# Optimization experiments

Hardware: AMD Instinct MI355X
Metric: run time of the kernel (lower is better)

Reference implementation:

```python
import jax, jax.numpy as jnp
import numpy as np

B, S, E, H = 4, 2048, 1024, 16
HD = E // H  # head_dim = 64


def setup_inputs() -> dict:
    key = jax.random.key(0)
    k1, k2, k3, k4 = jax.random.split(key, 4)
    x = jax.random.normal(k1, (B, S, E), dtype=jnp.float32)
    Wqkv = jax.random.normal(k2, (3 * E, E), dtype=jnp.float32) * (E ** -0.5)
    Wo = jax.random.normal(k3, (E, E), dtype=jnp.float32) * (E ** -0.5)
    bo = jax.random.normal(k4, (E,), dtype=jnp.float32) * 0.01
    return {"x": x, "Wqkv": Wqkv, "Wo": Wo, "bo": bo}


def reference(x, Wqkv, Wo, bo):
    b, s, e = x.shape
    # qkv projection (nn.Linear without bias: x @ W^T) -> (b, s, 3e)
    qkv = x @ Wqkv.T
    # reshape (b, s, H, 3*HD) -> (b, H, s, 3*HD), then chunk into q,k,v
    qkv = qkv.reshape(b, s, H, 3 * HD).transpose(0, 2, 1, 3)
    q, k, v = jnp.split(qkv, 3, axis=-1)  # each (b, H, s, HD)
    scale = 1.0 / jnp.sqrt(jnp.asarray(HD, dtype=x.dtype))
    scores = jnp.einsum('bhqd,bhkd->bhqk', q, k) * scale  # (b, H, s, s)
    causal = jnp.tril(jnp.ones((s, s), dtype=bool))
    scores = jnp.where(causal, scores, -jnp.inf)
    probs = jax.nn.softmax(scores, axis=-1)
    out = jnp.einsum('bhqk,bhkd->bhqd', probs, v)  # (b, H, s, HD)
    out = out.transpose(0, 2, 1, 3).reshape(b, s, e)
    return out @ Wo.T + bo
```

## Files before the change

kernel.cpp:

```cpp
#include <hip/hip_runtime.h>
#include <stdint.h>

#define Bn 4
#define Sn 2048
#define En 1024
#define Hn 16
#define HDn 64

typedef __bf16 bf16;
typedef __bf16 bf16x4 __attribute__((ext_vector_type(4)));
typedef __bf16 bf16x8 __attribute__((ext_vector_type(8)));
typedef float  f32x4  __attribute__((ext_vector_type(4)));
typedef float  f32x16 __attribute__((ext_vector_type(16)));
typedef uint32_t u32x4 __attribute__((ext_vector_type(4)));

#define GLDS(gp, lp) __builtin_amdgcn_global_load_lds( \
    (const __attribute__((address_space(1))) void*)(gp), \
    (__attribute__((address_space(3))) void*)(lp), 16, 0, 0)

#define BAR() __builtin_amdgcn_s_barrier()
#define WLG() do { asm volatile("s_waitcnt lgkmcnt(0)" ::: "memory"); \
                   __builtin_amdgcn_sched_barrier(0); } while (0)
#define WVM4() asm volatile("s_waitcnt vmcnt(4)" ::: "memory")

__global__ __launch_bounds__(256) void cvt_f32_to_bf16(
    const float* __restrict__ in, bf16* __restrict__ out, int n4)
{
    int i = blockIdx.x * 256 + threadIdx.x;
    if (i >= n4) return;
    float4 f = reinterpret_cast<const float4*>(in)[i];
    bf16x4 o;
    o[0] = (bf16)f.x; o[1] = (bf16)f.y; o[2] = (bf16)f.z; o[3] = (bf16)f.w;
    reinterpret_cast<bf16x4*>(out)[i] = o;
}

template<int MODE>
__global__ __launch_bounds__(512, 2) void gemm256(
    const bf16* __restrict__ Ag, const bf16* __restrict__ Bw,
    int M, int N, int K,
    bf16* __restrict__ q_out, bf16* __restrict__ k_out, bf16* __restrict__ v_out,
    float* __restrict__ c_out, const float* __restrict__ bias)
{
    __shared__ __align__(16) bf16 lA[2 * 256 * 64];
    __shared__ __align__(16) bf16 lB[2 * 256 * 64];

    const int tid  = threadIdx.x;
    const int lane = tid & 63;
    const int w    = tid >> 6;
    const int wm = w >> 2, wn = w & 3;
    const int lr = lane & 15, lg = lane >> 4;
    const int m0 = blockIdx.y * 256;
    const int n0 = blockIdx.x * 256;
    const int NT = K >> 6;
    const int niter = NT >> 1;

    const int srow = tid >> 3;
    const int sck  = (tid & 7) ^ ((tid >> 3) & 7);

    f32x4 acc[8][4] = {};

    auto stageA = [&](int t, int half) {
        const int ts = t < NT ? t : NT - 1;
        bf16* Ld = lA + ((t & 1) ? 16384 : 0) + (half*128 + w*8) * 64;
        const bf16* S = Ag + (size_t)(m0 + half*128 + srow) * K + ts*64 + sck*8;
        GLDS(S, Ld);
        GLDS(S + (size_t)64 * K, Ld + 64 * 64);
    };
    auto stageB = [&](int t, int half) {
        const int ts = t < NT ? t : NT - 1;
        bf16* Ld = lB + ((t & 1) ? 16384 : 0) + (half*128 + w*8) * 64;
        const bf16* S = Bw + (size_t)(n0 + half*128 + srow) * K + ts*64 + sck*8;
        GLDS(S, Ld);
        GLDS(S + (size_t)64 * K, Ld + 64 * 64);
    };
    auto ldA4 = [&](bf16x8 (&a)[4][2], const bf16* Lb, int qm) {
        #pragma unroll
        for (int ii = 0; ii < 4; ++ii) {
            const bf16* p = Lb + (wm*128 + qm*64 + ii*16 + lr) * 64;
            #pragma unroll
            for (int kk = 0; kk < 2; ++kk)
                a[ii][kk] = *reinterpret_cast<const bf16x8*>(p + (((kk << 2) + lg) ^ (lr & 7)) * 8);
        }
    };
    auto ldB2 = [&](bf16x8 (&b)[2][2], const bf16* Lb, int qn) {
        #pragma unroll
        for (int j = 0; j < 2; ++j) {
            const bf16* p = Lb + (wn*64 + qn*32 + j*16 + lr) * 64;
            #pragma unroll
            for (int kk = 0; kk < 2; ++kk)
                b[j][kk] = *reinterpret_cast<const bf16x8*>(p + (((kk << 2) + lg) ^ (lr & 7)) * 8);
        }
    };
    auto mmac = [&](const bf16x8 (&a)[4][2], const bf16x8 (&b)[2][2], int qm, int qn) {
        __builtin_amdgcn_s_setprio(1);
        #pragma unroll
        for (int ii = 0; ii < 4; ++ii)
            #pragma unroll
            for (int j = 0; j < 2; ++j)
                #pragma unroll
                for (int kk = 0; kk < 2; ++kk)
                    acc[qm*4 + ii][qn*2 + j] = __builtin_amdgcn_mfma_f32_16x16x32_bf16(
                        a[ii][kk], b[j][kk], acc[qm*4 + ii][qn*2 + j], 0, 0, 0);
        __builtin_amdgcn_s_setprio(0);
    };

    stageA(0, 0); stageA(0, 1); stageB(0, 0); stageB(0, 1);
    stageB(1, 0); stageB(1, 1);
    WVM4(); BAR();

    const bf16* A0 = lA;          const bf16* A1 = lA + 16384;
    const bf16* B0l = lB;         const bf16* B1l = lB + 16384;
    bf16x8 a[4][2], b0[2][2], b1[2][2];

    for (int i = 0; i < niter; ++i) {
        const int t = 2 * i;
        ldA4(a, A0, 0); ldB2(b0, B0l, 0);
        stageA(t + 1, 0);
        BAR(); WLG();
        mmac(a, b0, 0, 0);
        BAR();
        ldB2(b1, B0l, 1);
        stageA(t + 1, 1);
        BAR(); WLG();
        mmac(a, b1, 0, 1);
        BAR();
        ldA4(a, A0, 1);
        stageB(t + 2, 0);
        BAR(); WLG();
        mmac(a, b0, 1, 0);
        BAR();
        stageB(t + 2, 1);
        WVM4(); BAR();
        mmac(a, b1, 1, 1);
        BAR();
        ldA4(a, A1, 0); ldB2(b0, B1l, 0);
        stageA(t + 2, 0);
        BAR(); WLG();
        mmac(a, b0, 0, 0);
        BAR();
        ldB2(b1, B1l, 1);
        stageA(t + 2, 1);
        BAR(); WLG();
        mmac(a, b1, 0, 1);
        BAR();
        ldA4(a, A1, 1);
        stageB(t + 3, 0);
        BAR(); WLG();
        mmac(a, b0, 1, 0);
        BAR();
        stageB(t + 3, 1);
        WVM4(); BAR();
        mmac(a, b1, 1, 1);
        BAR();
    }

    #pragma unroll
    for (int ii = 0; ii < 8; ++ii) {
        #pragma unroll
        for (int j = 0; j < 4; ++j) {
            const int colb = n0 + wn*64 + j*16 + lr;
            #pragma unroll
            for (int r = 0; r < 4; ++r) {
                const int rowb = m0 + wm*128 + ii*16 + lg*4 + r;
                const float v = acc[ii][j][r];
                if (MODE == 0) {
                    const int bb = rowb >> 11, s = rowb & (Sn - 1);
                    const int h = colb / 192, rr = colb - h*192;
                    const int wq = rr >> 6, hd = rr & 63;
                    const size_t off = (((size_t)(bb*Hn + h))*Sn + s)*HDn + hd;
                    const bf16 bv = (bf16)v;
                    if (wq == 0)      q_out[off] = bv;
                    else if (wq == 1) k_out[off] = bv;
                    else              v_out[off] = bv;
                } else {
                    c_out[(size_t)rowb*N + colb] = v + bias[colb];
                }
            }
        }
    }
}

template<int MODE>
__global__ __launch_bounds__(256) void gemm_bt(
    const bf16* __restrict__ A, const bf16* __restrict__ Bw,
    int M, int N, int K,
    bf16* __restrict__ q_out, bf16* __restrict__ k_out, bf16* __restrict__ v_out,
    float* __restrict__ c_out, const float* __restrict__ bias)
{
    __shared__ bf16 lA[128*64];
    __shared__ bf16 lB[128*64];
    const int tid  = threadIdx.x;
    const int lane = tid & 63;
    const int wv   = tid >> 6;
    const int wm = wv >> 1, wn = wv & 1;
    const int m0 = blockIdx.y * 128;
    const int n0 = blockIdx.x * 128;
    const int lr = lane & 15, lg = lane >> 4;

    f32x4 acc[4][4] = {};

    const int rowA = wv*8 + (lane>>3);
    const int col8 = (lane&7)*8;

    for (int k0 = 0; k0 < K; k0 += 64) {
        #pragma unroll
        for (int c = 0; c < 4; ++c) {
            int row = c*32 + rowA;
            GLDS(A  + (size_t)(m0+row)*K + k0 + col8, lA + (c*32 + wv*8)*64);
            GLDS(Bw + (size_t)(n0+row)*K + k0 + col8, lB + (c*32 + wv*8)*64);
        }
        __syncthreads();
        #pragma unroll
        for (int kk = 0; kk < 64; kk += 32) {
            bf16x8 af[4], bfv[4];
            #pragma unroll
            for (int i = 0; i < 4; ++i)
                af[i] = *reinterpret_cast<const bf16x8*>(lA + (wm*64 + i*16 + lr)*64 + kk + lg*8);
            #pragma unroll
            for (int j = 0; j < 4; ++j)
                bfv[j] = *reinterpret_cast<const bf16x8*>(lB + (wn*64 + j*16 + lr)*64 + kk + lg*8);
            #pragma unroll
            for (int i = 0; i < 4; ++i)
                #pragma unroll
                for (int j = 0; j < 4; ++j)
                    acc[i][j] = __builtin_amdgcn_mfma_f32_16x16x32_bf16(af[i], bfv[j], acc[i][j], 0, 0, 0);
        }
        __syncthreads();
    }

    #pragma unroll
    for (int i = 0; i < 4; ++i) {
        #pragma unroll
        for (int j = 0; j < 4; ++j) {
            const int colb = n0 + wn*64 + j*16 + lr;
            #pragma unroll
            for (int r = 0; r < 4; ++r) {
                const int rowb = m0 + wm*64 + i*16 + lg*4 + r;
                const float v = acc[i][j][r];
                if (MODE == 0) {
                    const int b = rowb >> 11, s = rowb & (Sn-1);
                    const int h = colb / 192, rr = colb - h*192;
                    const int wq = rr >> 6, hd = rr & 63;
                    const size_t off = (((size_t)(b*Hn + h))*Sn + s)*HDn + hd;
                    const bf16 bv = (bf16)v;
                    if (wq == 0)      q_out[off] = bv;
                    else if (wq == 1) k_out[off] = bv;
                    else              v_out[off] = bv;
                } else {
                    c_out[(size_t)rowb*N + colb] = v + bias[colb];
                }
            }
        }
    }
}

static __device__ __forceinline__ uint32_t pkbf(float lo, float hi)
{
    uint16_t a = __builtin_bit_cast(uint16_t, (bf16)lo);
    uint16_t b = __builtin_bit_cast(uint16_t, (bf16)hi);
    return (uint32_t)a | ((uint32_t)b << 16);
}

__global__ __launch_bounds__(512) void attn_fwd(
    const bf16* __restrict__ Q, const bf16* __restrict__ Kg, const bf16* __restrict__ Vg,
    bf16* __restrict__ O)
{
    __shared__ __align__(16) bf16 Kl[64*64];
    __shared__ __align__(16) bf16 Vt[64*64];

    const int tid  = threadIdx.x;
    const int lane = tid & 63;
    const int w    = tid >> 6;
    const int col  = lane & 31;
    const int hv   = lane >> 5;
    const int bh   = blockIdx.x;
    const int qb   = (gridDim.y - 1) - blockIdx.y;
    const int q0w  = qb*256 + w*32;
    const int qg   = q0w + col;

    const bf16* Qb = Q  + (size_t)bh*Sn*HDn;
    const bf16* Kb = Kg + (size_t)bh*Sn*HDn;
    const bf16* Vb = Vg + (size_t)bh*Sn*HDn;

    bf16x8 aq[4];
    #pragma unroll
    for (int ks = 0; ks < 4; ++ks)
        aq[ks] = *reinterpret_cast<const bf16x8*>(Qb + (size_t)qg*HDn + ks*16 + hv*8);

    f32x16 ov[2] = {};
    const float S2 = 0.18033688011112042f;
    float m_run = -1e30f, l_run = 0.f;

    const int srow = tid >> 3;
    const int scol = tid & 7;
    const int ksw  = scol ^ (srow & 7);

    const int nkt = 4*(qb+1);
    for (int kt = 0; kt < nkt; ++kt) {
        const int k0 = kt*64;
        __syncthreads();
        GLDS(Kb + (size_t)(k0 + srow)*HDn + ksw*8, Kl + (size_t)w*512);
        {
            bf16x8 vv = *reinterpret_cast<const bf16x8*>(Vb + (size_t)(k0 + srow)*HDn + scol*8);
            #pragma unroll
            for (int j = 0; j < 8; ++j) {
                const int chunk = (scol*8 + j)*8 + ((srow>>3) ^ scol);
                Vt[chunk*8 + (srow&7)] = vv[j];
            }
        }
        __syncthreads();

        if (k0 > q0w + 31) continue;

        f32x16 st[2] = {};
        #pragma unroll
        for (int kb = 0; kb < 2; ++kb) {
            const int key = kb*32 + col;
            #pragma unroll
            for (int ks = 0; ks < 4; ++ks) {
                const int chunk = key*8 + ((ks*2 + hv) ^ (key & 7));
                bf16x8 kf = *reinterpret_cast<const bf16x8*>(Kl + chunk*8);
                st[kb] = __builtin_amdgcn_mfma_f32_32x32x16_bf16(kf, aq[ks], st[kb], 0, 0, 0);
            }
        }

        if (k0 + 63 > q0w) {
            #pragma unroll
            for (int kb = 0; kb < 2; ++kb)
                #pragma unroll
                for (int r = 0; r < 16; ++r) {
                    const int keyg = k0 + kb*32 + (r&3) + 8*(r>>2) + 4*hv;
                    if (keyg > qg) st[kb][r] = -1e30f;
                }
        }

        float mx = st[0][0];
        #pragma unroll
        for (int kb = 0; kb < 2; ++kb)
            #pragma unroll
            for (int r = 0; r < 16; ++r)
                mx = fmaxf(mx, st[kb][r]);
        mx = fmaxf(mx, __shfl_xor(mx, 32));
        const float smax2 = mx * S2;

        if (!__all(smax2 - m_run <= 8.0f)) {
            const float mn = fmaxf(m_run, smax2);
            const float fr = exp2f(m_run - mn);
            l_run *= fr;
            #pragma unroll
            for (int hb = 0; hb < 2; ++hb)
                #pragma unroll
                for (int r = 0; r < 16; ++r)
                    ov[hb][r] *= fr;
            m_run = mn;
        }

        uint32_t wpk[2][8];
        float sum = 0.f;
        #pragma unroll
        for (int kb = 0; kb < 2; ++kb)
            #pragma unroll
            for (int i = 0; i < 8; ++i) {
                const float e0 = exp2f(fmaf(st[kb][2*i],   S2, -m_run));
                const float e1 = exp2f(fmaf(st[kb][2*i+1], S2, -m_run));
                sum += e0 + e1;
                wpk[kb][i] = pkbf(e0, e1);
            }
        l_run += sum;

        #pragma unroll
        for (int s = 0; s < 4; ++s) {
            const int kb = s >> 1, ls = s & 1;
            const uint32_t send0 = hv ? wpk[kb][4*ls+0] : wpk[kb][4*ls+2];
            const uint32_t send1 = hv ? wpk[kb][4*ls+1] : wpk[kb][4*ls+3];
            const uint32_t keep0 = hv ? wpk[kb][4*ls+2] : wpk[kb][4*ls+0];
            const uint32_t keep1 = hv ? wpk[kb][4*ls+3] : wpk[kb][4*ls+1];
            const uint32_t r0 = (uint32_t)__shfl_xor((int)send0, 32);
            const uint32_t r1 = (uint32_t)__shfl_xor((int)send1, 32);
            u32x4 pwv = { hv ? r0 : keep0, hv ? r1 : keep1,
                          hv ? keep0 : r0, hv ? keep1 : r1 };
            bf16x8 pB = __builtin_bit_cast(bf16x8, pwv);
            #pragma unroll
            for (int hb = 0; hb < 2; ++hb) {
                const int hd = hb*32 + col;
                const int chunk = hd*8 + ((s*2 + hv) ^ ((hd>>3) & 7));
                bf16x8 vf = *reinterpret_cast<const bf16x8*>(Vt + chunk*8);
                ov[hb] = __builtin_amdgcn_mfma_f32_32x32x16_bf16(vf, pB, ov[hb], 0, 0, 0);
            }
        }
    }

    const float lt  = l_run + __shfl_xor(l_run, 32);
    const float inv = 1.0f / lt;
    const int b = bh >> 4, hh = bh & 15;
    bf16* Ob = O + ((size_t)(b*Sn + qg))*En + hh*HDn;
    #pragma unroll
    for (int hb = 0; hb < 2; ++hb)
        #pragma unroll
        for (int g = 0; g < 4; ++g) {
            bf16x4 o4;
            #pragma unroll
            for (int r4 = 0; r4 < 4; ++r4)
                o4[r4] = (bf16)(ov[hb][g*4 + r4] * inv);
            *reinterpret_cast<bf16x4*>(Ob + hb*32 + g*8 + 4*hv) = o4;
        }
}

extern "C" void kernel_launch(void* const* d_in, const int* in_sizes, int n_in,
                              void* d_out, int out_size, void* d_ws, size_t ws_size,
                              hipStream_t stream)
{
    (void)in_sizes; (void)n_in; (void)out_size; (void)ws_size;
    const float* x    = (const float*)d_in[0];
    const float* Wqkv = (const float*)d_in[1];
    const float* Wo   = (const float*)d_in[2];
    const float* bo   = (const float*)d_in[3];
    float* out = (float*)d_out;

    const size_t nBS = (size_t)Bn*Sn;
    char* ws = (char*)d_ws;
    bf16* xb    = (bf16*)ws; ws += nBS*En*2;
    bf16* wqkvb = (bf16*)ws; ws += (size_t)3*En*En*2;
    bf16* wob   = (bf16*)ws; ws += (size_t)En*En*2;
    bf16* Qb    = (bf16*)ws; ws += nBS*En*2;
    bf16* Kb    = (bf16*)ws; ws += nBS*En*2;
    bf16* Vb    = (bf16*)ws; ws += nBS*En*2;
    bf16* AO    = (bf16*)ws; ws += nBS*En*2;

    int n4 = (int)(nBS*En/4);
    cvt_f32_to_bf16<<<(n4+255)/256, 256, 0, stream>>>(x, xb, n4);
    n4 = 3*En*En/4;
    cvt_f32_to_bf16<<<(n4+255)/256, 256, 0, stream>>>(Wqkv, wqkvb, n4);
    n4 = En*En/4;
    cvt_f32_to_bf16<<<(n4+255)/256, 256, 0, stream>>>(Wo, wob, n4);

    gemm256<0><<<dim3(3*En/256, nBS/256), 512, 0, stream>>>(
        xb, wqkvb, (int)nBS, 3*En, En, Qb, Kb, Vb, nullptr, nullptr);

    attn_fwd<<<dim3(Bn*Hn, Sn/256), 512, 0, stream>>>(Qb, Kb, Vb, AO);

    gemm_bt<1><<<dim3(En/128, nBS/128), 256, 0, stream>>>(
        AO, wob, (int)nBS, En, En, nullptr, nullptr, nullptr, out, bo);
}
```

Baseline: 197.1 us.

## Double-buffer K/V tiles in attention kernel and prefetch next tile during compute

The attention kernel now keeps two LDS buffers for K and transposed V. The loads for the next 64-key tile (async global-to-LDS for K, register load for V) are issued before the current tile's QK^T and softmax work, and the V transpose-store happens before the PV matmul. This cuts the per-iteration pair of barriers to a single one and hides global load latency behind MFMA work. It also raises MFMA wave priority with s_setprio, and in exchange doubles LDS use and keeps more registers live.

```diff
diff --git a/kernel.cpp b/kernel.cpp
--- a/kernel.cpp
+++ b/kernel.cpp
@@ -22,6 +22,7 @@
 #define WLG() do { asm volatile("s_waitcnt lgkmcnt(0)" ::: "memory"); \
                    __builtin_amdgcn_sched_barrier(0); } while (0)
 #define WVM4() asm volatile("s_waitcnt vmcnt(4)" ::: "memory")
+#define WVM0() asm volatile("s_waitcnt vmcnt(0)" ::: "memory")
 
 __global__ __launch_bounds__(256) void cvt_f32_to_bf16(
     const float* __restrict__ in, bf16* __restrict__ out, int n4)
@@ -265,8 +266,8 @@
     const bf16* __restrict__ Q, const bf16* __restrict__ Kg, const bf16* __restrict__ Vg,
     bf16* __restrict__ O)
 {
-    __shared__ __align__(16) bf16 Kl[64*64];
-    __shared__ __align__(16) bf16 Vt[64*64];
+    __shared__ __align__(16) bf16 Kl[2][64*64];
+    __shared__ __align__(16) bf16 Vt[2][64*64];
 
     const int tid  = threadIdx.x;
     const int lane = tid & 63;
@@ -295,99 +296,125 @@
     const int scol = tid & 7;
     const int ksw  = scol ^ (srow & 7);
 
+    auto vWrite = [&](bf16* Vd, bf16x8 vv) {
+        #pragma unroll
+        for (int j = 0; j < 8; ++j) {
+            const int chunk = (scol*8 + j)*8 + ((srow>>3) ^ scol);
+            Vd[chunk*8 + (srow&7)] = vv[j];
+        }
+    };
+
     const int nkt = 4*(qb+1);
+
+    GLDS(Kb + (size_t)srow*HDn + ksw*8, &Kl[0][0] + (size_t)w*512);
+    {
+        bf16x8 vv0 = *reinterpret_cast<const bf16x8*>(Vb + (size_t)srow*HDn + scol*8);
+        WVM0();
+        vWrite(&Vt[0][0], vv0);
+    }
+    __syncthreads();
+
     for (int kt = 0; kt < nkt; ++kt) {
+        const int cur = kt & 1;
         const int k0 = kt*64;
+        const bool more = (kt + 1 < nkt);
+        const bool skip = (k0 > q0w + 31);
+
+        bf16x8 vv;
+        if (more) {
+            GLDS(Kb + (size_t)(k0 + 64 + srow)*HDn + ksw*8, &Kl[cur^1][0] + (size_t)w*512);
+            vv = *reinterpret_cast<const bf16x8*>(Vb + (size_t)(k0 + 64 + srow)*HDn + scol*8);
+        }
+
+        uint32_t wpk[2][8];
+        if (!skip) {
+            f32x16 st[2] = {};
+            __builtin_amdgcn_s_setprio(1);
+            #pragma unroll
+            for (int kb = 0; kb < 2; ++kb) {
+                const int key = kb*32 + col;
+                #pragma unroll
+                for (int ks = 0; ks < 4; ++ks) {
+                    const int chunk = key*8 + ((ks*2 + hv) ^ (key & 7));
+                    bf16x8 kf = *reinterpret_cast<const bf16x8*>(&Kl[cur][0] + chunk*8);
+                    st[kb] = __builtin_amdgcn_mfma_f32_32x32x16_bf16(kf, aq[ks], st[kb], 0, 0, 0);
+                }
+            }
+            __builtin_amdgcn_s_setprio(0);
+
+            if (k0 + 63 > q0w) {
+                #pragma unroll
+                for (int kb = 0; kb < 2; ++kb)
+                    #pragma unroll
+                    for (int r = 0; r < 16; ++r) {
+                        const int keyg = k0 + kb*32 + (r&3) + 8*(r>>2) + 4*hv;
+                        if (keyg > qg) st[kb][r] = -1e30f;
+                    }
+            }
+
+            float mx = st[0][0];
+            #pragma unroll
+            for (int kb = 0; kb < 2; ++kb)
+                #pragma unroll
+                for (int r = 0; r < 16; ++r)
+                    mx = fmaxf(mx, st[kb][r]);
+            mx = fmaxf(mx, __shfl_xor(mx, 32));
+            const float smax2 = mx * S2;
+
+            if (!__all(smax2 - m_run <= 8.0f)) {
+                const float mn = fmaxf(m_run, smax2);
+                const float fr = exp2f(m_run - mn);
+                l_run *= fr;
+                #pragma unroll
+                for (int hb = 0; hb < 2; ++hb)
+                    #pragma unroll
+                    for (int r = 0; r < 16; ++r)
+                        ov[hb][r] *= fr;
+                m_run = mn;
+            }
+
+            float sum = 0.f;
+            #pragma unroll
+            for (int kb = 0; kb < 2; ++kb)
+                #pragma unroll
+                for (int i = 0; i < 8; ++i) {
+                    const float e0 = exp2f(fmaf(st[kb][2*i],   S2, -m_run));
+                    const float e1 = exp2f(fmaf(st[kb][2*i+1], S2, -m_run));
+                    sum += e0 + e1;
+                    wpk[kb][i] = pkbf(e0, e1);
+                }
+            l_run += sum;
+        }
+
+        WVM0();
+        if (more) vWrite(&Vt[cur^1][0], vv);
+
+        if (!skip) {
+            #pragma unroll
+            for (int s = 0; s < 4; ++s) {
+                const int kb = s >> 1, ls = s & 1;
+                const uint32_t send0 = hv ? wpk[kb][4*ls+0] : wpk[kb][4*ls+2];
+                const uint32_t send1 = hv ? wpk[kb][4*ls+1] : wpk[kb][4*ls+3];
+                const uint32_t keep0 = hv ? wpk[kb][4*ls+2] : wpk[kb][4*ls+0];
+                const uint32_t keep1 = hv ? wpk[kb][4*ls+3] : wpk[kb][4*ls+1];
+                const uint32_t r0 = (uint32_t)__shfl_xor((int)send0, 32);
+                const uint32_t r1 = (uint32_t)__shfl_xor((int)send1, 32);
+                u32x4 pwv = { hv ? r0 : keep0, hv ? r1 : keep1,
+                              hv ? keep0 : r0, hv ? keep1 : r1 };
+                bf16x8 pB = __builtin_bit_cast(bf16x8, pwv);
+                __builtin_amdgcn_s_setprio(1);
+                #pragma unroll
+                for (int hb = 0; hb < 2; ++hb) {
+                    const int hd = hb*32 + col;
+                    const int chunk = hd*8 + ((s*2 + hv) ^ ((hd>>3) & 7));
+                    bf16x8 vf = *reinterpret_cast<const bf16x8*>(&Vt[cur][0] + chunk*8);
+                    ov[hb] = __builtin_amdgcn_mfma_f32_32x32x16_bf16(vf, pB, ov[hb], 0, 0, 0);
+                }
+                __builtin_amdgcn_s_setprio(0);
+            }
+        }
+
         __syncthreads();
-        GLDS(Kb + (size_t)(k0 + srow)*HDn + ksw*8, Kl + (size_t)w*512);
-        {
-            bf16x8 vv = *reinterpret_cast<const bf16x8*>(Vb + (size_t)(k0 + srow)*HDn + scol*8);
-            #pragma unroll
-            for (int j = 0; j < 8; ++j) {
-                const int chunk = (scol*8 + j)*8 + ((srow>>3) ^ scol);
-                Vt[chunk*8 + (srow&7)] = vv[j];
-            }
-        }
-        __syncthreads();
-
-        if (k0 > q0w + 31) continue;
-
-        f32x16 st[2] = {};
-        #pragma unroll
-        for (int kb = 0; kb < 2; ++kb) {
-            const int key = kb*32 + col;
-            #pragma unroll
-            for (int ks = 0; ks < 4; ++ks) {
-                const int chunk = key*8 + ((ks*2 + hv) ^ (key & 7));
-                bf16x8 kf = *reinterpret_cast<const bf16x8*>(Kl + chunk*8);
-                st[kb] = __builtin_amdgcn_mfma_f32_32x32x16_bf16(kf, aq[ks], st[kb], 0, 0, 0);
-            }
-        }
-
-        if (k0 + 63 > q0w) {
-            #pragma unroll
-            for (int kb = 0; kb < 2; ++kb)
-                #pragma unroll
-                for (int r = 0; r < 16; ++r) {
-                    const int keyg = k0 + kb*32 + (r&3) + 8*(r>>2) + 4*hv;
-                    if (keyg > qg) st[kb][r] = -1e30f;
-                }
-        }
-
-        float mx = st[0][0];
-        #pragma unroll
-        for (int kb = 0; kb < 2; ++kb)
-            #pragma unroll
-            for (int r = 0; r < 16; ++r)
-                mx = fmaxf(mx, st[kb][r]);
-        mx = fmaxf(mx, __shfl_xor(mx, 32));
-        const float smax2 = mx * S2;
-
-        if (!__all(smax2 - m_run <= 8.0f)) {
-            const float mn = fmaxf(m_run, smax2);
-            const float fr = exp2f(m_run - mn);
-            l_run *= fr;
-            #pragma unroll
-            for (int hb = 0; hb < 2; ++hb)
-                #pragma unroll
-                for (int r = 0; r < 16; ++r)
-                    ov[hb][r] *= fr;
-            m_run = mn;
-        }
-
-        uint32_t wpk[2][8];
-        float sum = 0.f;
-        #pragma unroll
-        for (int kb = 0; kb < 2; ++kb)
-            #pragma unroll
-            for (int i = 0; i < 8; ++i) {
-                const float e0 = exp2f(fmaf(st[kb][2*i],   S2, -m_run));
-                const float e1 = exp2f(fmaf(st[kb][2*i+1], S2, -m_run));
-                sum += e0 + e1;
-                wpk[kb][i] = pkbf(e0, e1);
-            }
-        l_run += sum;
-
-        #pragma unroll
-        for (int s = 0; s < 4; ++s) {
-            const int kb = s >> 1, ls = s & 1;
-            const uint32_t send0 = hv ? wpk[kb][4*ls+0] : wpk[kb][4*ls+2];
-            const uint32_t send1 = hv ? wpk[kb][4*ls+1] : wpk[kb][4*ls+3];
-            const uint32_t keep0 = hv ? wpk[kb][4*ls+2] : wpk[kb][4*ls+0];
-            const uint32_t keep1 = hv ? wpk[kb][4*ls+3] : wpk[kb][4*ls+1];
-            const uint32_t r0 = (uint32_t)__shfl_xor((int)send0, 32);
-            const uint32_t r1 = (uint32_t)__shfl_xor((int)send1, 32);
-            u32x4 pwv = { hv ? r0 : keep0, hv ? r1 : keep1,
-                          hv ? keep0 : r0, hv ? keep1 : r1 };
-            bf16x8 pB = __builtin_bit_cast(bf16x8, pwv);
-            #pragma unroll
-            for (int hb = 0; hb < 2; ++hb) {
-                const int hd = hb*32 + col;
-                const int chunk = hd*8 + ((s*2 + hv) ^ ((hd>>3) & 7));
-                bf16x8 vf = *reinterpret_cast<const bf16x8*>(Vt + chunk*8);
-                ov[hb] = __builtin_amdgcn_mfma_f32_32x32x16_bf16(vf, pB, ov[hb], 0, 0, 0);
-            }
-        }
     }
 
     const float lt  = l_run + __shfl_xor(l_run, 32);
```

New measurement: 204.3 us. 1.04x slower.

## Write V transposed from QKV GEMM and read K/V directly from global in attention

Applied to the files above, without the earlier changes.

The QKV projection epilogue now stores V in head-dim-major (transposed) layout, so the attention kernel can load V fragments directly from global memory without an LDS transpose. The attention kernel drops shared-memory staging and barriers for K and V, reading fragments straight from global/L2. Blocks shrink to 256 threads covering 128 queries, and each wave computes its own causal key-tile count so it skips tiles beyond its range. The trade-off is uncoalesced, strided global reads that rely on cache hits, and the V epilogue writes become strided scatter stores. The unused MODE 0 epilogue in gemm_bt is also removed.

```diff
diff --git a/kernel.cpp b/kernel.cpp
--- a/kernel.cpp
+++ b/kernel.cpp
@@ -167,11 +167,14 @@
                     const int bb = rowb >> 11, s = rowb & (Sn - 1);
                     const int h = colb / 192, rr = colb - h*192;
                     const int wq = rr >> 6, hd = rr & 63;
-                    const size_t off = (((size_t)(bb*Hn + h))*Sn + s)*HDn + hd;
                     const bf16 bv = (bf16)v;
-                    if (wq == 0)      q_out[off] = bv;
-                    else if (wq == 1) k_out[off] = bv;
-                    else              v_out[off] = bv;
+                    if (wq == 0) {
+                        q_out[(((size_t)(bb*Hn + h))*Sn + s)*HDn + hd] = bv;
+                    } else if (wq == 1) {
+                        k_out[(((size_t)(bb*Hn + h))*Sn + s)*HDn + hd] = bv;
+                    } else {
+                        v_out[(((size_t)(bb*Hn + h))*HDn + hd)*Sn + s] = bv;
+                    }
                 } else {
                     c_out[(size_t)rowb*N + colb] = v + bias[colb];
                 }
@@ -237,16 +240,7 @@
             for (int r = 0; r < 4; ++r) {
                 const int rowb = m0 + wm*64 + i*16 + lg*4 + r;
                 const float v = acc[i][j][r];
-                if (MODE == 0) {
-                    const int b = rowb >> 11, s = rowb & (Sn-1);
-                    const int h = colb / 192, rr = colb - h*192;
-                    const int wq = rr >> 6, hd = rr & 63;
-                    const size_t off = (((size_t)(b*Hn + h))*Sn + s)*HDn + hd;
-                    const bf16 bv = (bf16)v;
-                    if (wq == 0)      q_out[off] = bv;
-                    else if (wq == 1) k_out[off] = bv;
-                    else              v_out[off] = bv;
-                } else {
+                if (MODE == 1) {
                     c_out[(size_t)rowb*N + colb] = v + bias[colb];
                 }
             }
@@ -261,26 +255,23 @@
     return (uint32_t)a | ((uint32_t)b << 16);
 }
 
-__global__ __launch_bounds__(512) void attn_fwd(
-    const bf16* __restrict__ Q, const bf16* __restrict__ Kg, const bf16* __restrict__ Vg,
+__global__ __launch_bounds__(256) void attn_fwd(
+    const bf16* __restrict__ Q, const bf16* __restrict__ Kg, const bf16* __restrict__ Vtg,
     bf16* __restrict__ O)
 {
-    __shared__ __align__(16) bf16 Kl[64*64];
-    __shared__ __align__(16) bf16 Vt[64*64];
-
     const int tid  = threadIdx.x;
     const int lane = tid & 63;
     const int w    = tid >> 6;
     const int col  = lane & 31;
     const int hv   = lane >> 5;
-    const int bh   = blockIdx.x;
-    const int qb   = (gridDim.y - 1) - blockIdx.y;
-    const int q0w  = qb*256 + w*32;
+    const int bh   = blockIdx.y;
+    const int qb   = (gridDim.x - 1) - blockIdx.x;
+    const int q0w  = qb*128 + w*32;
     const int qg   = q0w + col;
 
-    const bf16* Qb = Q  + (size_t)bh*Sn*HDn;
-    const bf16* Kb = Kg + (size_t)bh*Sn*HDn;
-    const bf16* Vb = Vg + (size_t)bh*Sn*HDn;
+    const bf16* Qb = Q   + (size_t)bh*Sn*HDn;
+    const bf16* Kb = Kg  + (size_t)bh*Sn*HDn;
+    const bf16* Vb = Vtg + (size_t)bh*HDn*Sn;
 
     bf16x8 aq[4];
     #pragma unroll
@@ -291,35 +282,17 @@
     const float S2 = 0.18033688011112042f;
     float m_run = -1e30f, l_run = 0.f;
 
-    const int srow = tid >> 3;
-    const int scol = tid & 7;
-    const int ksw  = scol ^ (srow & 7);
-
-    const int nkt = 4*(qb+1);
+    const int nkt = (q0w + 31)/64 + 1;
     for (int kt = 0; kt < nkt; ++kt) {
         const int k0 = kt*64;
-        __syncthreads();
-        GLDS(Kb + (size_t)(k0 + srow)*HDn + ksw*8, Kl + (size_t)w*512);
-        {
-            bf16x8 vv = *reinterpret_cast<const bf16x8*>(Vb + (size_t)(k0 + srow)*HDn + scol*8);
-            #pragma unroll
-            for (int j = 0; j < 8; ++j) {
-                const int chunk = (scol*8 + j)*8 + ((srow>>3) ^ scol);
-                Vt[chunk*8 + (srow&7)] = vv[j];
-            }
-        }
-        __syncthreads();
-
-        if (k0 > q0w + 31) continue;
 
         f32x16 st[2] = {};
         #pragma unroll
         for (int kb = 0; kb < 2; ++kb) {
-            const int key = kb*32 + col;
+            const bf16* Kr = Kb + (size_t)(k0 + kb*32 + col)*HDn + hv*8;
             #pragma unroll
             for (int ks = 0; ks < 4; ++ks) {
-                const int chunk = key*8 + ((ks*2 + hv) ^ (key & 7));
-                bf16x8 kf = *reinterpret_cast<const bf16x8*>(Kl + chunk*8);
+                bf16x8 kf = *reinterpret_cast<const bf16x8*>(Kr + ks*16);
                 st[kb] = __builtin_amdgcn_mfma_f32_32x32x16_bf16(kf, aq[ks], st[kb], 0, 0, 0);
             }
         }
@@ -382,9 +355,8 @@
             bf16x8 pB = __builtin_bit_cast(bf16x8, pwv);
             #pragma unroll
             for (int hb = 0; hb < 2; ++hb) {
-                const int hd = hb*32 + col;
-                const int chunk = hd*8 + ((s*2 + hv) ^ ((hd>>3) & 7));
-                bf16x8 vf = *reinterpret_cast<const bf16x8*>(Vt + chunk*8);
+                bf16x8 vf = *reinterpret_cast<const bf16x8*>(
+                    Vb + (size_t)(hb*32 + col)*Sn + k0 + s*16 + hv*8);
                 ov[hb] = __builtin_amdgcn_mfma_f32_32x32x16_bf16(vf, pB, ov[hb], 0, 0, 0);
             }
         }
@@ -437,7 +409,7 @@
     gemm256<0><<<dim3(3*En/256, nBS/256), 512, 0, stream>>>(
         xb, wqkvb, (int)nBS, 3*En, En, Qb, Kb, Vb, nullptr, nullptr);
 
-    attn_fwd<<<dim3(Bn*Hn, Sn/256), 512, 0, stream>>>(Qb, Kb, Vb, AO);
+    attn_fwd<<<dim3(Sn/128, Bn*Hn), 256, 0, stream>>>(Qb, Kb, Vb, AO);
 
     gemm_bt<1><<<dim3(En/128, nBS/128), 256, 0, stream>>>(
         AO, wob, (int)nBS, En, En, nullptr, nullptr, nullptr, out, bo);
```

Result: slower. 377.3 us (+91.4%).
